# Kernel tuning notes

Hardware: AMD Instinct MI355X
Metric: run time of the kernel (lower is better)

## Reference

```python
import jax, jax.numpy as jnp
import numpy as np

# Static multi-level pyramid: sum(H*W) = 21760 = Len
SRC_SHAPES = ((128, 128), (64, 64), (32, 32), (16, 16))


def _bilinear_sample(v_flat, H, W, x, y):
    """F.grid_sample(mode='bilinear', padding_mode='zeros', align_corners=False).
    v_flat: (BH, D, H*W); x, y: (BH, QP) pixel-space coords. Returns (BH, D, QP)."""
    x0 = jnp.floor(x)
    y0 = jnp.floor(y)
    x0i = x0.astype(jnp.int32)
    y0i = y0.astype(jnp.int32)
    wx1 = x - x0
    wy1 = y - y0
    out = jnp.zeros((v_flat.shape[0], v_flat.shape[1], x.shape[1]), dtype=v_flat.dtype)
    for dy, wy in ((0, 1.0 - wy1), (1, wy1)):
        for dx, wx in ((0, 1.0 - wx1), (1, wx1)):
            xi = x0i + dx
            yi = y0i + dy
            valid = (xi >= 0) & (xi < W) & (yi >= 0) & (yi < H)
            idx = jnp.clip(yi, 0, H - 1) * W + jnp.clip(xi, 0, W - 1)
            g = jnp.take_along_axis(v_flat, idx[:, None, :], axis=2)  # (BH, D, QP)
            w = (wx * wy * valid.astype(v_flat.dtype))[:, None, :]
            out = out + g * w
    return out


def setup_inputs() -> dict:
    key = jax.random.key(0)
    k1, k2, k3 = jax.random.split(key, 3)
    B, nH, D, Q, L, P = 2, 8, 32, 21760, 4, 4
    Len = sum(h * w for h, w in SRC_SHAPES)
    assert Len == Q
    value = jax.random.normal(k1, (B, Len, nH, D), dtype=jnp.float32)
    sampling_locations = jax.random.uniform(k2, (B, Q, nH, L, P, 2), dtype=jnp.float32)
    attention_weights = jax.nn.softmax(
        jax.random.normal(k3, (B, Q, nH, L * P), dtype=jnp.float32), axis=-1
    ).reshape(B, Q, nH, L, P)
    shapes = jnp.asarray(np.array(SRC_SHAPES, dtype=np.int64))
    starts = jnp.asarray(np.concatenate([[0], np.cumsum([h * w for h, w in SRC_SHAPES])[:-1]]).astype(np.int64))
    return {
        "value": value,
        "value_spatial_shapes": shapes,
        "value_level_start_index": starts,
        "sampling_locations": sampling_locations,
        "attention_weights": attention_weights,
        "im2col_step": 64,
    }


def reference(value, value_spatial_shapes, value_level_start_index, sampling_locations, attention_weights, im2col_step):
    B, Len, nH, D = value.shape
    Q = sampling_locations.shape[1]
    L = len(SRC_SHAPES)
    P = sampling_locations.shape[4]
    # (B, Len, H, D) -> (B*H, D, Len)
    v = jnp.transpose(value, (0, 2, 3, 1)).reshape(B * nH, D, Len)
    # normalized [0,1] locations -> grid_sample [-1,1] coords
    grids = 2.0 * sampling_locations - 1.0  # (B, Q, H, L, P, 2)
    grids = jnp.transpose(grids, (0, 2, 1, 3, 4, 5)).reshape(B * nH, Q, L, P, 2)
    aw = jnp.transpose(attention_weights, (0, 2, 1, 3, 4)).reshape(B * nH, 1, Q, L, P)
    out = jnp.zeros((B * nH, D, Q), dtype=value.dtype)
    start = 0
    for lvl, (H, W) in enumerate(SRC_SHAPES):
        v_l = v[:, :, start : start + H * W]  # (BH, D, H*W), static slice
        g = grids[:, :, lvl].reshape(B * nH, Q * P, 2)
        # align_corners=False mapping from [-1,1] to pixel coords
        x = ((g[..., 0] + 1.0) * W - 1.0) * 0.5
        y = ((g[..., 1] + 1.0) * H - 1.0) * 0.5
        s = _bilinear_sample(v_l, H, W, x, y).reshape(B * nH, D, Q, P)
        out = out + (s * aw[:, :, :, lvl]).sum(-1)
        start += H * W
    # (BH, D, Q) -> (B, Q, H*D)
    return jnp.transpose(out.reshape(B, nH * D, Q), (0, 2, 1))
```

## Files before the change

### kernel.cpp

```cpp
#include <hip/hip_runtime.h>
#include <hip/hip_fp16.h>


namespace {
constexpr int kB    = 2;
constexpr int kQ    = 21760;
constexpr int kHd   = 8;
constexpr int kD    = 32;
constexpr int kLen  = 21760;
constexpr int kRow  = kHd * kD;
constexpr int kQBlk = 64;
constexpr int kBlksPerPair = kQ / kQBlk;
constexpr int kS3   = 21504;
constexpr size_t kValElems = (size_t)kB * kLen * kRow;
}

__device__ __forceinline__ void fma4(float4& a, float w, const float4 v) {
    a.x = fmaf(w, v.x, a.x);
    a.y = fmaf(w, v.y, a.y);
    a.z = fmaf(w, v.z, a.z);
    a.w = fmaf(w, v.w, a.w);
}

__device__ __forceinline__ void fma8h(float* acc, float w, uint4 u) {
    const __half* hp = (const __half*)&u;
    #pragma unroll
    for (int e = 0; e < 8; ++e)
        acc[e] = fmaf(w, __half2float(hp[e]), acc[e]);
}

__global__ __launch_bounds__(256) void cvt_t(
    const float* __restrict__ in, __half* __restrict__ outh)
{
    const int t   = blockIdx.x * 256 + threadIdx.x;
    const int sub = t & 7;
    const int h   = (t >> 3) & 7;
    const int bp  = t >> 6;
    const int b   = (bp >= kLen) ? 1 : 0;
    const int pix = bp - b * kLen;

    const float4 v = ((const float4*)in)[(size_t)bp * 64 + h * 8 + sub];
    __half2 h0 = __floats2half2_rn(v.x, v.y);
    __half2 h1 = __floats2half2_rn(v.z, v.w);
    uint2 u;
    u.x = *(unsigned*)&h0;
    u.y = *(unsigned*)&h1;
    ((uint2*)outh)[((size_t)(b * kHd + h) * kLen + pix) * 8 + sub] = u;
}

__global__ __launch_bounds__(256, 4) void msda_fwd_h(
    const __half* __restrict__ vh,
    const float* __restrict__ loc,
    const float* __restrict__ attw,
    float* __restrict__ out)
{
    const int i    = blockIdx.x;
    const int xcd  = i & 7;
    const int k    = i >> 3;
    const int b    = (k >= kBlksPerPair) ? 1 : 0;
    const int j    = k - b * kBlksPerPair;
    const int h    = xcd;

    const char* slice = (const char*)vh + ((size_t)(b * kHd + h) * kLen) * 64;

    __shared__ __align__(16) char lv3[256 * 64];
    {
        const uint4* src = (const uint4*)(slice + (size_t)kS3 * 64);
        uint4* dst = (uint4*)lv3;
        #pragma unroll
        for (int r = 0; r < 4; ++r)
            dst[r * 256 + threadIdx.x] = src[r * 256 + threadIdx.x];
    }
    __syncthreads();

    const int qi   = threadIdx.x >> 2;
    const int sub  = threadIdx.x & 3;
    const int q    = j * kQBlk + qi;
    const int g    = (b * kQ + q) * kHd + h;

    const float4* lp4 = (const float4*)(loc  + (size_t)g * 32);
    const float4* ap4 = (const float4*)(attw + (size_t)g * 16);
    const char* vthr = slice + sub * 16;

    float acc[8];
    #pragma unroll
    for (int e = 0; e < 8; ++e) acc[e] = 0.f;

    constexpr int Hs[3] = {128, 64, 32};
    constexpr int Ws[3] = {128, 64, 32};
    constexpr int Ss[3] = {0, 16384, 20480};

    #pragma unroll
    for (int l = 0; l < 3; ++l) {
        const int W = Ws[l];
        const int H = Hs[l];
        const int S = Ss[l];

        const float4 lc0 = lp4[2 * l];
        const float4 lc1 = lp4[2 * l + 1];
        const float4 av  = ap4[l];

        const float lx[4] = {lc0.x, lc0.z, lc1.x, lc1.z};
        const float ly[4] = {lc0.y, lc0.w, lc1.y, lc1.w};
        const float aa[4] = {av.x,  av.y,  av.z,  av.w};

        #pragma unroll
        for (int p = 0; p < 4; ++p) {
            const float x = fmaf(lx[p], (float)W, -0.5f);
            const float y = fmaf(ly[p], (float)H, -0.5f);
            const float x0f = floorf(x);
            const float y0f = floorf(y);
            const float fx = x - x0f;
            const float fy = y - y0f;
            const int   x0 = (int)x0f;
            const int   y0 = (int)y0f;
            const float a  = aa[p];

            const bool vx0 = (unsigned)x0       < (unsigned)W;
            const bool vx1 = (unsigned)(x0 + 1) < (unsigned)W;
            const bool vy0 = (unsigned)y0       < (unsigned)H;
            const bool vy1 = (unsigned)(y0 + 1) < (unsigned)H;

            const int xc0 = min(max(x0, 0),     W - 1);
            const int xc1 = min(max(x0 + 1, 0), W - 1);
            const int yc0 = min(max(y0, 0),     H - 1);
            const int yc1 = min(max(y0 + 1, 0), H - 1);

            float w00 = a * (1.f - fx) * (1.f - fy);
            float w01 = a * fx * (1.f - fy);
            float w10 = a * (1.f - fx) * fy;
            float w11 = a * fx * fy;
            w00 = (vy0 && vx0) ? w00 : 0.f;
            w01 = (vy0 && vx1) ? w01 : 0.f;
            w10 = (vy1 && vx0) ? w10 : 0.f;
            w11 = (vy1 && vx1) ? w11 : 0.f;

            const int r0 = (S + yc0 * W) << 6;
            const int r1 = (S + yc1 * W) << 6;
            const uint4 v00 = *(const uint4*)(vthr + r0 + (xc0 << 6));
            const uint4 v01 = *(const uint4*)(vthr + r0 + (xc1 << 6));
            const uint4 v10 = *(const uint4*)(vthr + r1 + (xc0 << 6));
            const uint4 v11 = *(const uint4*)(vthr + r1 + (xc1 << 6));

            fma8h(acc, w00, v00);
            fma8h(acc, w01, v01);
            fma8h(acc, w10, v10);
            fma8h(acc, w11, v11);
        }
    }

    {
        constexpr int W = 16, H = 16;
        const float4 lc0 = lp4[6];
        const float4 lc1 = lp4[7];
        const float4 av  = ap4[3];

        const float lx[4] = {lc0.x, lc0.z, lc1.x, lc1.z};
        const float ly[4] = {lc0.y, lc0.w, lc1.y, lc1.w};
        const float aa[4] = {av.x,  av.y,  av.z,  av.w};

        const char* lthr = lv3 + sub * 16;

        #pragma unroll
        for (int p = 0; p < 4; ++p) {
            const float x = fmaf(lx[p], (float)W, -0.5f);
            const float y = fmaf(ly[p], (float)H, -0.5f);
            const float x0f = floorf(x);
            const float y0f = floorf(y);
            const float fx = x - x0f;
            const float fy = y - y0f;
            const int   x0 = (int)x0f;
            const int   y0 = (int)y0f;
            const float a  = aa[p];

            const bool vx0 = (unsigned)x0       < (unsigned)W;
            const bool vx1 = (unsigned)(x0 + 1) < (unsigned)W;
            const bool vy0 = (unsigned)y0       < (unsigned)H;
            const bool vy1 = (unsigned)(y0 + 1) < (unsigned)H;

            const int xc0 = min(max(x0, 0),     W - 1);
            const int xc1 = min(max(x0 + 1, 0), W - 1);
            const int yc0 = min(max(y0, 0),     H - 1);
            const int yc1 = min(max(y0 + 1, 0), H - 1);

            float w00 = a * (1.f - fx) * (1.f - fy);
            float w01 = a * fx * (1.f - fy);
            float w10 = a * (1.f - fx) * fy;
            float w11 = a * fx * fy;
            w00 = (vy0 && vx0) ? w00 : 0.f;
            w01 = (vy0 && vx1) ? w01 : 0.f;
            w10 = (vy1 && vx0) ? w10 : 0.f;
            w11 = (vy1 && vx1) ? w11 : 0.f;

            const uint4 v00 = *(const uint4*)(lthr + ((yc0 * W + xc0) << 6));
            const uint4 v01 = *(const uint4*)(lthr + ((yc0 * W + xc1) << 6));
            const uint4 v10 = *(const uint4*)(lthr + ((yc1 * W + xc0) << 6));
            const uint4 v11 = *(const uint4*)(lthr + ((yc1 * W + xc1) << 6));

            fma8h(acc, w00, v00);
            fma8h(acc, w01, v01);
            fma8h(acc, w10, v10);
            fma8h(acc, w11, v11);
        }
    }

    float* op = out + ((size_t)(b * kQ + q)) * kRow + h * kD + sub * 8;
    float4 r0, r1;
    r0.x = acc[0]; r0.y = acc[1]; r0.z = acc[2]; r0.w = acc[3];
    r1.x = acc[4]; r1.y = acc[5]; r1.z = acc[6]; r1.w = acc[7];
    ((float4*)op)[0] = r0;
    ((float4*)op)[1] = r1;
}

__global__ __launch_bounds__(256, 4) void msda_fwd_f32(
    const float* __restrict__ value,
    const float* __restrict__ loc,
    const float* __restrict__ attw,
    float* __restrict__ out)
{
    const int i    = blockIdx.x;
    const int xcd  = i & 7;
    const int k    = i >> 3;
    const int bpp  = kQ / 32;
    const int b    = (k >= bpp) ? 1 : 0;
    const int j    = k - b * bpp;
    const int h    = xcd;

    __shared__ float lv3[256 * kD];
    {
        const float* src = value + ((size_t)(b * kLen + kS3)) * kRow + h * kD;
        float4* dst = (float4*)lv3;
        #pragma unroll
        for (int r = 0; r < 8; ++r) {
            const int idx  = r * 256 + threadIdx.x;
            const int pix  = idx >> 3;
            const int quad = idx & 7;
            dst[idx] = *(const float4*)(src + (size_t)pix * kRow + quad * 4);
        }
    }
    __syncthreads();

    const int qi   = threadIdx.x >> 3;
    const int sub  = threadIdx.x & 7;
    const int q    = j * 32 + qi;
    const int g    = (b * kQ + q) * kHd + h;

    const float4* lp4 = (const float4*)(loc  + (size_t)g * 32);
    const float4* ap4 = (const float4*)(attw + (size_t)g * 16);
    const float*  vb  = value + (size_t)b * kLen * kRow + h * kD + sub * 4;

    float4 acc = make_float4(0.f, 0.f, 0.f, 0.f);

    constexpr int Hs[3] = {128, 64, 32};
    constexpr int Ws[3] = {128, 64, 32};
    constexpr int Ss[3] = {0, 16384, 20480};

    #pragma unroll
    for (int l = 0; l < 3; ++l) {
        const int W = Ws[l];
        const int H = Hs[l];
        const int S = Ss[l];

        const float4 lc0 = lp4[2 * l];
        const float4 lc1 = lp4[2 * l + 1];
        const float4 av  = ap4[l];

        const float lx[4] = {lc0.x, lc0.z, lc1.x, lc1.z};
        const float ly[4] = {lc0.y, lc0.w, lc1.y, lc1.w};
        const float aa[4] = {av.x,  av.y,  av.z,  av.w};

        #pragma unroll
        for (int p = 0; p < 4; ++p) {
            const float x = fmaf(lx[p], (float)W, -0.5f);
            const float y = fmaf(ly[p], (float)H, -0.5f);
            const float x0f = floorf(x);
            const float y0f = floorf(y);
            const float fx = x - x0f;
            const float fy = y - y0f;
            const int   x0 = (int)x0f;
            const int   y0 = (int)y0f;
            const float a  = aa[p];

            const bool vx0 = (unsigned)x0       < (unsigned)W;
            const bool vx1 = (unsigned)(x0 + 1) < (unsigned)W;
            const bool vy0 = (unsigned)y0       < (unsigned)H;
            const bool vy1 = (unsigned)(y0 + 1) < (unsigned)H;

            const int xc0 = min(max(x0, 0),     W - 1);
            const int xc1 = min(max(x0 + 1, 0), W - 1);
            const int yc0 = min(max(y0, 0),     H - 1);
            const int yc1 = min(max(y0 + 1, 0), H - 1);

            float w00 = a * (1.f - fx) * (1.f - fy);
            float w01 = a * fx * (1.f - fy);
            float w10 = a * (1.f - fx) * fy;
            float w11 = a * fx * fy;
            w00 = (vy0 && vx0) ? w00 : 0.f;
            w01 = (vy0 && vx1) ? w01 : 0.f;
            w10 = (vy1 && vx0) ? w10 : 0.f;
            w11 = (vy1 && vx1) ? w11 : 0.f;

            const int r0 = (S + yc0 * W) * kRow;
            const int r1 = (S + yc1 * W) * kRow;
            const float4 v00 = *(const float4*)(vb + r0 + xc0 * kRow);
            const float4 v01 = *(const float4*)(vb + r0 + xc1 * kRow);
            const float4 v10 = *(const float4*)(vb + r1 + xc0 * kRow);
            const float4 v11 = *(const float4*)(vb + r1 + xc1 * kRow);

            fma4(acc, w00, v00);
            fma4(acc, w01, v01);
            fma4(acc, w10, v10);
            fma4(acc, w11, v11);
        }
    }

    {
        constexpr int W = 16, H = 16;
        const float4 lc0 = lp4[6];
        const float4 lc1 = lp4[7];
        const float4 av  = ap4[3];

        const float lx[4] = {lc0.x, lc0.z, lc1.x, lc1.z};
        const float ly[4] = {lc0.y, lc0.w, lc1.y, lc1.w};
        const float aa[4] = {av.x,  av.y,  av.z,  av.w};

        #pragma unroll
        for (int p = 0; p < 4; ++p) {
            const float x = fmaf(lx[p], (float)W, -0.5f);
            const float y = fmaf(ly[p], (float)H, -0.5f);
            const float x0f = floorf(x);
            const float y0f = floorf(y);
            const float fx = x - x0f;
            const float fy = y - y0f;
            const int   x0 = (int)x0f;
            const int   y0 = (int)y0f;
            const float a  = aa[p];

            const bool vx0 = (unsigned)x0       < (unsigned)W;
            const bool vx1 = (unsigned)(x0 + 1) < (unsigned)W;
            const bool vy0 = (unsigned)y0       < (unsigned)H;
            const bool vy1 = (unsigned)(y0 + 1) < (unsigned)H;

            const int xc0 = min(max(x0, 0),     W - 1);
            const int xc1 = min(max(x0 + 1, 0), W - 1);
            const int yc0 = min(max(y0, 0),     H - 1);
            const int yc1 = min(max(y0 + 1, 0), H - 1);

            float w00 = a * (1.f - fx) * (1.f - fy);
            float w01 = a * fx * (1.f - fy);
            float w10 = a * (1.f - fx) * fy;
            float w11 = a * fx * fy;
            w00 = (vy0 && vx0) ? w00 : 0.f;
            w01 = (vy0 && vx1) ? w01 : 0.f;
            w10 = (vy1 && vx0) ? w10 : 0.f;
            w11 = (vy1 && vx1) ? w11 : 0.f;

            const float* lbase = lv3 + sub * 4;
            const float4 v00 = *(const float4*)(lbase + (yc0 * W + xc0) * kD);
            const float4 v01 = *(const float4*)(lbase + (yc0 * W + xc1) * kD);
            const float4 v10 = *(const float4*)(lbase + (yc1 * W + xc0) * kD);
            const float4 v11 = *(const float4*)(lbase + (yc1 * W + xc1) * kD);

            fma4(acc, w00, v00);
            fma4(acc, w01, v01);
            fma4(acc, w10, v10);
            fma4(acc, w11, v11);
        }
    }

    *(float4*)(out + ((size_t)(b * kQ + q)) * kRow + h * kD + sub * 4) = acc;
}

extern "C" void kernel_launch(void* const* d_in, const int* in_sizes, int n_in,
                              void* d_out, int out_size, void* d_ws, size_t ws_size,
                              hipStream_t stream) {
    const float* value = (const float*)d_in[0];
    const float* loc   = (const float*)d_in[3];
    const float* attw  = (const float*)d_in[4];
    float* out = (float*)d_out;

    if (ws_size >= kValElems * sizeof(__half)) {
        __half* vh = (__half*)d_ws;
        const int nthr = (int)(kValElems / 4);
        cvt_t<<<nthr / 256, 256, 0, stream>>>(value, vh);
        const int grid = kB * kHd * kBlksPerPair;
        msda_fwd_h<<<grid, 256, 0, stream>>>(vh, loc, attw, out);
    } else {
        const int grid = kB * kHd * (kQ / 32);
        msda_fwd_f32<<<grid, 256, 0, stream>>>(value, loc, attw, out);
    }
}
```

Before: 94.40 us.

## Pad fp16 value maps with zero border to remove bilinear bounds checks

Converts the value tensor to fp16 in a per-(batch,head) layout where each pyramid level has a one-pixel zero border, so bilinear corner fetches need no validity masks or clamps. The new kernel reads four corners unconditionally, with each thread handling 8 channels, and keeps the smallest level in LDS. This adds a memset of the padded workspace and a larger workspace requirement, and it assumes sampling locations stay within [0,1].

```diff
diff --git a/kernel.cpp b/kernel.cpp
--- a/kernel.cpp
+++ b/kernel.cpp
@@ -13,6 +13,10 @@
 constexpr int kBlksPerPair = kQ / kQBlk;
 constexpr int kS3   = 21504;
 constexpr size_t kValElems = (size_t)kB * kLen * kRow;
+
+constexpr int kPadPx    = 22736;
+constexpr int kSp[4]    = {0, 16900, 21256, 22412};
+constexpr size_t kPadBytes = (size_t)kB * kHd * kPadPx * 64;
 }
 
 __device__ __forceinline__ void fma4(float4& a, float w, const float4 v) {
@@ -27,6 +31,180 @@
     #pragma unroll
     for (int e = 0; e < 8; ++e)
         acc[e] = fmaf(w, __half2float(hp[e]), acc[e]);
+}
+
+__global__ __launch_bounds__(256) void cvt_pad(
+    const float* __restrict__ in, __half* __restrict__ outh)
+{
+    const int t   = blockIdx.x * 256 + threadIdx.x;
+    const int sub = t & 7;
+    const int h   = (t >> 3) & 7;
+    const int bp  = t >> 6;
+    const int b   = (bp >= kLen) ? 1 : 0;
+    const int pix = bp - b * kLen;
+
+    int pidx;
+    if (pix < 16384) {
+        pidx = ((pix >> 7) + 1) * 130 + (pix & 127) + 1;
+    } else if (pix < 20480) {
+        const int r = pix - 16384;
+        pidx = 16900 + ((r >> 6) + 1) * 66 + (r & 63) + 1;
+    } else if (pix < 21504) {
+        const int r = pix - 20480;
+        pidx = 21256 + ((r >> 5) + 1) * 34 + (r & 31) + 1;
+    } else {
+        const int r = pix - 21504;
+        pidx = 22412 + ((r >> 4) + 1) * 18 + (r & 15) + 1;
+    }
+
+    const float4 v = ((const float4*)in)[(size_t)bp * 64 + h * 8 + sub];
+    __half2 h0 = __floats2half2_rn(v.x, v.y);
+    __half2 h1 = __floats2half2_rn(v.z, v.w);
+    uint2 u;
+    u.x = *(unsigned*)&h0;
+    u.y = *(unsigned*)&h1;
+    ((uint2*)outh)[((size_t)(b * kHd + h) * kPadPx + pidx) * 8 + sub] = u;
+}
+
+__global__ __launch_bounds__(256, 4) void msda_fwd_hp(
+    const __half* __restrict__ vh,
+    const float* __restrict__ loc,
+    const float* __restrict__ attw,
+    float* __restrict__ out)
+{
+    const int i    = blockIdx.x;
+    const int xcd  = i & 7;
+    const int k    = i >> 3;
+    const int b    = (k >= kBlksPerPair) ? 1 : 0;
+    const int j    = k - b * kBlksPerPair;
+    const int h    = xcd;
+
+    const char* slice = (const char*)vh
+                      + ((size_t)(b * kHd + h) * kPadPx) * 64;
+
+    __shared__ __align__(16) char lv3[324 * 64];
+    {
+        const uint4* src = (const uint4*)(slice + (size_t)kSp[3] * 64);
+        uint4* dst = (uint4*)lv3;
+        #pragma unroll
+        for (int r = 0; r < 6; ++r) {
+            const int idx = r * 256 + threadIdx.x;
+            if (idx < 324 * 4) dst[idx] = src[idx];
+        }
+    }
+    __syncthreads();
+
+    const int qi   = threadIdx.x >> 2;
+    const int sub  = threadIdx.x & 3;
+    const int q    = j * kQBlk + qi;
+    const int g    = (b * kQ + q) * kHd + h;
+
+    const float4* lp4 = (const float4*)(loc  + (size_t)g * 32);
+    const float4* ap4 = (const float4*)(attw + (size_t)g * 16);
+    const char* vthr = slice + sub * 16;
+
+    float acc[8];
+    #pragma unroll
+    for (int e = 0; e < 8; ++e) acc[e] = 0.f;
+
+    constexpr int   Wd[3] = {128, 64, 32};
+    constexpr int   Wp[3] = {130, 66, 34};
+
+    #pragma unroll
+    for (int l = 0; l < 3; ++l) {
+        const float Wf = (float)Wd[l];
+        const int   Ws = Wp[l];
+        const int   Sp = kSp[l];
+
+        const float4 lc0 = lp4[2 * l];
+        const float4 lc1 = lp4[2 * l + 1];
+        const float4 av  = ap4[l];
+
+        const float lx[4] = {lc0.x, lc0.z, lc1.x, lc1.z};
+        const float ly[4] = {lc0.y, lc0.w, lc1.y, lc1.w};
+        const float aa[4] = {av.x,  av.y,  av.z,  av.w};
+
+        #pragma unroll
+        for (int p = 0; p < 4; ++p) {
+            const float x = fmaf(lx[p], Wf, 0.5f);
+            const float y = fmaf(ly[p], Wf, 0.5f);
+            const float x0f = floorf(x);
+            const float y0f = floorf(y);
+            const float fx = x - x0f;
+            const float fy = y - y0f;
+            const int   x0 = (int)x0f;
+            const int   y0 = (int)y0f;
+            const float a  = aa[p];
+
+            const float awy1 = a * fy;
+            const float awy0 = a - awy1;
+            const float w11  = awy1 * fx;
+            const float w10  = awy1 - w11;
+            const float w01  = awy0 * fx;
+            const float w00  = awy0 - w01;
+
+            const char* pb = vthr + ((Sp + y0 * Ws + x0) << 6);
+            const uint4 v00 = *(const uint4*)(pb);
+            const uint4 v01 = *(const uint4*)(pb + 64);
+            const uint4 v10 = *(const uint4*)(pb + Ws * 64);
+            const uint4 v11 = *(const uint4*)(pb + Ws * 64 + 64);
+
+            fma8h(acc, w00, v00);
+            fma8h(acc, w01, v01);
+            fma8h(acc, w10, v10);
+            fma8h(acc, w11, v11);
+        }
+    }
+
+    {
+        const float4 lc0 = lp4[6];
+        const float4 lc1 = lp4[7];
+        const float4 av  = ap4[3];
+
+        const float lx[4] = {lc0.x, lc0.z, lc1.x, lc1.z};
+        const float ly[4] = {lc0.y, lc0.w, lc1.y, lc1.w};
+        const float aa[4] = {av.x,  av.y,  av.z,  av.w};
+
+        const char* lthr = lv3 + sub * 16;
+
+        #pragma unroll
+        for (int p = 0; p < 4; ++p) {
+            const float x = fmaf(lx[p], 16.f, 0.5f);
+            const float y = fmaf(ly[p], 16.f, 0.5f);
+            const float x0f = floorf(x);
+            const float y0f = floorf(y);
+            const float fx = x - x0f;
+            const float fy = y - y0f;
+            const int   x0 = (int)x0f;
+            const int   y0 = (int)y0f;
+            const float a  = aa[p];
+
+            const float awy1 = a * fy;
+            const float awy0 = a - awy1;
+            const float w11  = awy1 * fx;
+            const float w10  = awy1 - w11;
+            const float w01  = awy0 * fx;
+            const float w00  = awy0 - w01;
+
+            const char* pb = lthr + ((y0 * 18 + x0) << 6);
+            const uint4 v00 = *(const uint4*)(pb);
+            const uint4 v01 = *(const uint4*)(pb + 64);
+            const uint4 v10 = *(const uint4*)(pb + 18 * 64);
+            const uint4 v11 = *(const uint4*)(pb + 18 * 64 + 64);
+
+            fma8h(acc, w00, v00);
+            fma8h(acc, w01, v01);
+            fma8h(acc, w10, v10);
+            fma8h(acc, w11, v11);
+        }
+    }
+
+    float* op = out + ((size_t)(b * kQ + q)) * kRow + h * kD + sub * 8;
+    float4 r0, r1;
+    r0.x = acc[0]; r0.y = acc[1]; r0.z = acc[2]; r0.w = acc[3];
+    r1.x = acc[4]; r1.y = acc[5]; r1.z = acc[6]; r1.w = acc[7];
+    ((float4*)op)[0] = r0;
+    ((float4*)op)[1] = r1;
 }
 
 __global__ __launch_bounds__(256) void cvt_t(
@@ -379,14 +557,20 @@
     const float* attw  = (const float*)d_in[4];
     float* out = (float*)d_out;
 
-    if (ws_size >= kValElems * sizeof(__half)) {
+    const int nthr = (int)(kValElems / 4);
+    const int grid = kB * kHd * kBlksPerPair;
+
+    if (ws_size >= kPadBytes) {
         __half* vh = (__half*)d_ws;
-        const int nthr = (int)(kValElems / 4);
+        hipMemsetAsync(d_ws, 0, kPadBytes, stream);
+        cvt_pad<<<nthr / 256, 256, 0, stream>>>(value, vh);
+        msda_fwd_hp<<<grid, 256, 0, stream>>>(vh, loc, attw, out);
+    } else if (ws_size >= kValElems * sizeof(__half)) {
+        __half* vh = (__half*)d_ws;
         cvt_t<<<nthr / 256, 256, 0, stream>>>(value, vh);
-        const int grid = kB * kHd * kBlksPerPair;
         msda_fwd_h<<<grid, 256, 0, stream>>>(vh, loc, attw, out);
     } else {
-        const int grid = kB * kHd * (kQ / 32);
-        msda_fwd_f32<<<grid, 256, 0, stream>>>(value, loc, attw, out);
-    }
-}
+        const int grid32 = kB * kHd * (kQ / 32);
+        msda_fwd_f32<<<grid32, 256, 0, stream>>>(value, loc, attw, out);
+    }
+}
```

New measurement: 113.6 us. 20.3% more time.
